# Kernel optimization log

Measured on AMD Instinct MI355X. Metric: run time of the kernel, lower is better.

## Reference

```python
import jax, jax.numpy as jnp
import numpy as np

D_MODEL = 1024
N_HEADS = 16
HEAD_DIM = D_MODEL // N_HEADS
HIDDEN = 4096
EPS = 1e-5


def setup_inputs() -> dict:
    key = jax.random.key(0)
    ks = jax.random.split(key, 16)
    s = 1.0 / np.sqrt(D_MODEL)
    sh = 1.0 / np.sqrt(HIDDEN)
    inp = {
        'x': jax.random.normal(ks[0], (4, 2048, D_MODEL), dtype=jnp.float32),
        'Wq': jax.random.normal(ks[1], (D_MODEL, D_MODEL), dtype=jnp.float32) * s,
        'bq': jnp.zeros((D_MODEL,), jnp.float32),
        'Wk': jax.random.normal(ks[2], (D_MODEL, D_MODEL), dtype=jnp.float32) * s,
        'bk': jnp.zeros((D_MODEL,), jnp.float32),
        'Wv': jax.random.normal(ks[3], (D_MODEL, D_MODEL), dtype=jnp.float32) * s,
        'bv': jnp.zeros((D_MODEL,), jnp.float32),
        'Wo': jax.random.normal(ks[4], (D_MODEL, D_MODEL), dtype=jnp.float32) * s,
        'bo': jnp.zeros((D_MODEL,), jnp.float32),
        'gamma1': jnp.ones((D_MODEL,), jnp.float32),
        'beta1': jnp.zeros((D_MODEL,), jnp.float32),
        'W1': jax.random.normal(ks[5], (D_MODEL, HIDDEN), dtype=jnp.float32) * s,
        'b1': jnp.zeros((HIDDEN,), jnp.float32),
        'W2': jax.random.normal(ks[6], (HIDDEN, D_MODEL), dtype=jnp.float32) * sh,
        'b2': jnp.zeros((D_MODEL,), jnp.float32),
        'gamma2': jnp.ones((D_MODEL,), jnp.float32),
        'beta2': jnp.zeros((D_MODEL,), jnp.float32),
    }
    return inp


def _layernorm(x, gamma, beta):
    mu = jnp.mean(x, axis=-1, keepdims=True)
    var = jnp.mean(jnp.square(x - mu), axis=-1, keepdims=True)
    return (x - mu) * jax.lax.rsqrt(var + EPS) * gamma + beta


def _encoder_layer(x, Wq, bq, Wk, bk, Wv, bv, Wo, bo, gamma1, beta1,
                   W1, b1, W2, b2, gamma2, beta2):
    B, S, _ = x.shape
    # projections -> [B, H, S, Dh]
    def split_heads(t):
        return t.reshape(B, S, N_HEADS, HEAD_DIM).transpose(0, 2, 1, 3)
    q = split_heads(x @ Wq + bq)
    k = split_heads(x @ Wk + bk)
    v = split_heads(x @ Wv + bv)
    scale = 1.0 / jnp.sqrt(jnp.float32(HEAD_DIM))
    scores = jnp.einsum('bhqd,bhkd->bhqk', q, k) * scale
    attn = jax.nn.softmax(scores, axis=-1)
    ctx = jnp.einsum('bhqk,bhkd->bhqd', attn, v)
    ctx = ctx.transpose(0, 2, 1, 3).reshape(B, S, D_MODEL)
    attn_out = ctx @ Wo + bo
    # post-norm residual 1
    h = _layernorm(x + attn_out, gamma1, beta1)
    # MLP with exact (erf) GELU, as torch F.gelu default
    mlp = jax.nn.gelu(h @ W1 + b1, approximate=False) @ W2 + b2
    return _layernorm(h + mlp, gamma2, beta2)


def reference(x, Wq, bq, Wk, bk, Wv, bv, Wo, bo, gamma1, beta1,
              W1, b1, W2, b2, gamma2, beta2):
    return _encoder_layer(x, Wq, bq, Wk, bk, Wv, bv, Wo, bo, gamma1, beta1,
                          W1, b1, W2, b2, gamma2, beta2)
```

## Files before the change

kernel.cpp:

```cpp
#include <hip/hip_runtime.h>
#include <cstdint>
#include <cstddef>

using u16 = unsigned short;
using bf16x8 = __attribute__((ext_vector_type(8))) short;
using f32x4  = __attribute__((ext_vector_type(4))) float;

__device__ __forceinline__ u16 f2bf(float f) {
    union { float f; unsigned u; } v; v.f = f;
    unsigned r = v.u + 0x7fffu + ((v.u >> 16) & 1u);
    return (u16)(r >> 16);
}

__device__ __forceinline__ float bf2f(u16 b) {
    union { unsigned u; float f; } v; v.u = (unsigned)b << 16;
    return v.f;
}

__device__ __forceinline__ unsigned cvtpk(float lo, float hi) {
    unsigned r;
    asm("v_cvt_pk_bf16_f32 %0, %1, %2" : "=v"(r) : "v"(lo), "v"(hi));
    return r;
}

__device__ __forceinline__ float fexp2(float x) {
    float r;
    asm("v_exp_f32 %0, %1" : "=v"(r) : "v"(x));
    return r;
}

__device__ __forceinline__ float gelu_f(float x) {
    const float t2 = fminf(x * fmaf(0.10294825f, x * x, 2.3022082f), 80.f);
    const float e  = fexp2(t2);
    return x * e * __frcp_rn(e + 1.0f);
}

__device__ __forceinline__ void gld_lds16(const void* g, void* l) {
    __builtin_amdgcn_global_load_lds(
        (__attribute__((address_space(1))) void*)g,
        (__attribute__((address_space(3))) void*)l, 16, 0, 0);
}

__device__ __forceinline__ f32x4 mfma16(bf16x8 a, bf16x8 b, f32x4 c) {
    return __builtin_amdgcn_mfma_f32_16x16x32_bf16(a, b, c, 0, 0, 0);
}

__global__ __launch_bounds__(256)
void cast_kernel(const float* __restrict__ in, u16* __restrict__ out, int n8) {
    int i = blockIdx.x * 256 + threadIdx.x;
    if (i >= n8) return;
    const float4* p = (const float4*)in;
    float4 a = p[i * 2], b = p[i * 2 + 1];
    ushort4 r0 = make_ushort4(f2bf(a.x), f2bf(a.y), f2bf(a.z), f2bf(a.w));
    ushort4 r1 = make_ushort4(f2bf(b.x), f2bf(b.y), f2bf(b.z), f2bf(b.w));
    ((ushort4*)out)[i * 2]     = r0;
    ((ushort4*)out)[i * 2 + 1] = r1;
}

__global__ __launch_bounds__(256)
void tcast_all_kernel(const float* __restrict__ Wq, const float* __restrict__ Wk,
                      const float* __restrict__ Wv, const float* __restrict__ Wo,
                      const float* __restrict__ W1, const float* __restrict__ W2,
                      u16* __restrict__ wqkvt, u16* __restrict__ wot,
                      u16* __restrict__ w1t, u16* __restrict__ w2t)
{
    const int g = blockIdx.x;
    const float* src; u16* dst; int K, N, ti; float scale = 1.0f;
    if (g < 1024)      { src = Wq; dst = wqkvt;               K = 1024; N = 1024; ti = g;        scale = 0.18033688011112042f; }
    else if (g < 2048) { src = Wk; dst = wqkvt + 1048576;     K = 1024; N = 1024; ti = g - 1024; }
    else if (g < 3072) { src = Wv; dst = wqkvt + 2097152;     K = 1024; N = 1024; ti = g - 2048; }
    else if (g < 4096) { src = Wo; dst = wot;                 K = 1024; N = 1024; ti = g - 3072; }
    else if (g < 8192) { src = W1; dst = w1t;                 K = 1024; N = 4096; ti = g - 4096; }
    else               { src = W2; dst = w2t;                 K = 4096; N = 1024; ti = g - 8192; }
    const int nt = N >> 5;
    const int bx = ti % nt, by = ti / nt;
    const int k0 = by * 32, n0 = bx * 32;

    __shared__ float tile[32][33];
    const int tx = threadIdx.x & 31, ty = threadIdx.x >> 5;
    #pragma unroll
    for (int r = 0; r < 4; ++r) {
        int k = ty * 4 + r;
        tile[k][tx] = src[(size_t)(k0 + k) * N + n0 + tx];
    }
    __syncthreads();
    const int kx = (threadIdx.x & 15) * 2;
    const int ny = threadIdx.x >> 4;
    #pragma unroll
    for (int r = 0; r < 2; ++r) {
        const int n = ny * 2 + r;
        ushort2 o = make_ushort2(f2bf(tile[kx][n] * scale),
                                 f2bf(tile[kx + 1][n] * scale));
        *(ushort2*)&dst[(size_t)(n0 + n) * K + k0 + kx] = o;
    }
}

__global__ __launch_bounds__(256)
void bias_concat_kernel(const float* __restrict__ bq, const float* __restrict__ bk,
                        const float* __restrict__ bv, float* __restrict__ out) {
    int i = blockIdx.x * 256 + threadIdx.x;
    if (i >= 3072) return;
    float v;
    if (i < 1024)      v = bq[i] * 0.18033688011112042f;
    else if (i < 2048) v = bk[i - 1024];
    else               v = bv[i - 2048];
    out[i] = v;
}

template <int BM, int EPI>
__global__ __launch_bounds__(512, 1)
void gemm_pipe_kernel(const u16* __restrict__ A, const u16* __restrict__ Bt,
                      const float* __restrict__ bias, void* __restrict__ Cout,
                      int M, int N, int K)
{
    constexpr int AH  = BM * 64;
    constexpr int BH  = 16384;
    constexpr int BUF = 2 * AH + 2 * BH;
    constexpr int LPA = BM / 128;
    constexpr int GRP = LPA + 2;
    constexpr int MR  = BM / 32;

    extern __shared__ char smem[];

    const int tid  = threadIdx.x;
    const int wid  = tid >> 6, lane = tid & 63;
    const int l15  = lane & 15, l4 = lane >> 4;
    const int wm   = wid >> 2, wn = wid & 3;

    const int nwg = gridDim.x;
    const int qx = nwg >> 3, rx = nwg & 7;
    const int orig = blockIdx.x;
    const int xcd = orig & 7, jx = orig >> 3;
    const int wgid = (xcd < rx ? xcd * (qx + 1) : rx * (qx + 1) + (xcd - rx) * qx) + jx;
    const int NTn = N / 256;
    const int m0 = (wgid / NTn) * BM;
    const int n0 = (wgid % NTn) * 256;

    const int q0 = tid >> 3, g0 = tid & 7;
    const int u0 = g0 ^ (q0 & 7);
    const int r0 = (q0 << 1) | (u0 >> 2), c80 = u0 & 3;
    const int q1 = q0 + 64;
    const int u1 = g0 ^ (q1 & 7);
    const int r1 = (q1 << 1) | (u1 >> 2), c81 = u1 & 3;
    const u16* aP0 = A  + (size_t)(m0 + r0) * K + c80 * 8;
    const u16* aP1 = A  + (size_t)(m0 + r1) * K + c81 * 8;
    const u16* bP0 = Bt + (size_t)(n0 + r0) * K + c80 * 8;
    const u16* bP1 = Bt + (size_t)(n0 + r1) * K + c81 * 8;
    const int NT = K >> 6;
    const int NTm1 = NT - 1;

    auto stageAB = [&](int tt, int kk, int sb) {
        const int kte = (tt << 6) + (kk << 5);
        char* da = smem + sb * BUF + kk * AH + tid * 16;
        gld_lds16(aP0 + kte, da);
        if constexpr (LPA == 2) gld_lds16(aP1 + kte, da + 8192);
        char* db = smem + sb * BUF + 2 * AH + kk * BH + tid * 16;
        gld_lds16(bP0 + kte, db);
        gld_lds16(bP1 + kte, db + 8192);
    };

    auto frag_off = [&](int row) -> int {
        const int q = row >> 1;
        const int u = ((row & 1) << 2) | l4;
        const int g = u ^ (q & 7);
        return q * 128 + g * 16;
    };

    f32x4 acc[MR][4];
    #pragma unroll
    for (int i = 0; i < MR; ++i)
        #pragma unroll
        for (int jj = 0; jj < 4; ++jj) acc[i][jj] = f32x4{0.f, 0.f, 0.f, 0.f};

    stageAB(0, 0, 0); stageAB(0, 1, 0); stageAB(1, 0, 1);
    if constexpr (GRP == 4) asm volatile("s_waitcnt vmcnt(8)" ::: "memory");
    else                    asm volatile("s_waitcnt vmcnt(6)" ::: "memory");
    __builtin_amdgcn_s_barrier();
    asm volatile("" ::: "memory");

    for (int t = 0; t < NT; ++t) {
        const char* buf = smem + (t & 1) * BUF;
        bf16x8 bfr[4], af[MR];

        #pragma unroll
        for (int kk = 0; kk < 2; ++kk) {
            #pragma unroll
            for (int fc = 0; fc < 4; ++fc)
                bfr[fc] = *(const bf16x8*)(buf + 2 * AH + kk * BH +
                                           frag_off(wn * 64 + fc * 16 + l15));
            #pragma unroll
            for (int i = 0; i < MR; ++i)
                af[i] = *(const bf16x8*)(buf + kk * AH +
                                         frag_off(wm * (BM / 2) + i * 16 + l15));
            if (kk == 0) {
                const int tt = (t + 1 <= NTm1) ? t + 1 : NTm1;
                stageAB(tt, 1, (t + 1) & 1);
            } else {
                const int tt = (t + 2 <= NTm1) ? t + 2 : NTm1;
                stageAB(tt, 0, t & 1);
            }
            if constexpr (GRP == 4) asm volatile("s_waitcnt vmcnt(8)" ::: "memory");
            else                    asm volatile("s_waitcnt vmcnt(6)" ::: "memory");
            __builtin_amdgcn_s_barrier();
            asm volatile("" ::: "memory");
            __builtin_amdgcn_s_setprio(1);
            #pragma unroll
            for (int i = 0; i < MR; ++i)
                #pragma unroll
                for (int fc = 0; fc < 4; ++fc)
                    acc[i][fc] = mfma16(af[i], bfr[fc], acc[i][fc]);
            __builtin_amdgcn_s_setprio(0);
            asm volatile("" ::: "memory");
        }
    }

    float bv[4];
    #pragma unroll
    for (int fc = 0; fc < 4; ++fc) bv[fc] = bias[n0 + wn * 64 + fc * 16 + l15];
    #pragma unroll
    for (int fr = 0; fr < MR; ++fr) {
        const int rowg = m0 + wm * (BM / 2) + fr * 16 + l4 * 4;
        #pragma unroll
        for (int fc = 0; fc < 4; ++fc) {
            const int colg = n0 + wn * 64 + fc * 16 + l15;
            #pragma unroll
            for (int r = 0; r < 4; ++r) {
                const float v = acc[fr][fc][r] + bv[fc];
                const size_t off = (size_t)(rowg + r) * N + colg;
                if (EPI == 0) ((u16*)Cout)[off] = f2bf(v);
                else          ((u16*)Cout)[off] = f2bf(gelu_f(v));
            }
        }
    }
}

__global__ __launch_bounds__(256)
void vtrans_kernel(const u16* __restrict__ QKV, u16* __restrict__ Vt) {
    __shared__ u16 tile[64][68];
    const int t  = threadIdx.x;
    const int st = blockIdx.x, bh = blockIdx.y;
    const int b  = bh >> 4, h = bh & 15;
    #pragma unroll
    for (int i = 0; i < 2; ++i) {
        int sl = i * 32 + (t >> 3);
        const u16* gp = QKV + ((size_t)b * 2048 + st * 64 + sl) * 3072 + 2048 + h * 64 + (t & 7) * 8;
        ushort4 a = *(const ushort4*)gp;
        ushort4 c = *(const ushort4*)(gp + 4);
        u16* lp = &tile[sl][(t & 7) * 8];
        *(ushort4*)lp       = a;
        *(ushort4*)(lp + 4) = c;
    }
    __syncthreads();
    #pragma unroll
    for (int i = 0; i < 2; ++i) {
        int d  = i * 32 + (t >> 3);
        int s8 = (t & 7) * 8;
        ushort4 o0, o1;
        o0.x = tile[s8 + 0][d]; o0.y = tile[s8 + 1][d]; o0.z = tile[s8 + 2][d]; o0.w = tile[s8 + 3][d];
        o1.x = tile[s8 + 4][d]; o1.y = tile[s8 + 5][d]; o1.z = tile[s8 + 6][d]; o1.w = tile[s8 + 7][d];
        u16* op = Vt + ((size_t)bh * 64 + d) * 2048 + st * 64 + s8;
        *(ushort4*)op       = o0;
        *(ushort4*)(op + 4) = o1;
    }
}

__global__ __launch_bounds__(512)
void attn_kernel(const u16* __restrict__ QKV, const u16* __restrict__ Vt,
                 u16* __restrict__ ctx)
{
    __shared__ u16 smem[24576];

    const int tid = threadIdx.x;
    const int wid = tid >> 6, lane = tid & 63;
    const int l15 = lane & 15, l4 = lane >> 4;
    const int sw  = l15 & 7;
    const int lr  = lane >> 3;
    const int gsrc = ((lane & 7) ^ lr) * 8;
    const int g   = blockIdx.x;
    const int bh  = (g & 7) | ((g >> 6) << 3);
    const int qt  = (g >> 3) & 7;
    const int b = bh >> 4, h = bh & 15;
    const size_t qrow0 = (size_t)b * 2048 + (size_t)qt * 256;

    u16* const K0 = smem + 16384;
    u16* const V0 = smem + 20480;
    u16* const K1 = smem;
    u16* const V1 = smem + 4096;

    const u16* Qbase = QKV + h * 64;
    const u16* Kbase = QKV + (size_t)b * 2048 * 3072 + 1024 + h * 64;
    const u16* Vbase = Vt + (size_t)bh * 64 * 2048;

    #pragma unroll
    for (int c = 0; c < 4; ++c) {
        const int chunk = wid * 4 + c;
        const int row = chunk * 8 + lr;
        gld_lds16(Qbase + (qrow0 + row) * 3072 + gsrc,
                  (char*)smem + chunk * 1024);
    }

    auto stage_kv = [&](int kt, u16* kb, u16* vb) {
        const int rho = wid * 8 + lr;
        const int krow = (rho & 32) + ((rho & 16) >> 2) + ((rho & 12) << 1) + (rho & 3);
        gld_lds16(Kbase + (size_t)(kt + krow) * 3072 + gsrc,
                  (char*)kb + wid * 1024);
        gld_lds16(Vbase + (size_t)rho * 2048 + kt + gsrc,
                  (char*)vb + wid * 1024);
    };

    stage_kv(0, K0, V0);
    __syncthreads();

    bf16x8 qf[2][2];
    #pragma unroll
    for (int mi = 0; mi < 2; ++mi)
        #pragma unroll
        for (int kk = 0; kk < 2; ++kk)
            qf[mi][kk] = *(const bf16x8*)
                &smem[(size_t)(wid * 32 + mi * 16 + l15) * 64 + (((kk * 4 + l4) ^ sw) * 8)];
    __syncthreads();

    f32x4 accO[2][4] = {};
    f32x4 accL[2] = {};
    const short one_bf = (short)0x3F80;
    const bf16x8 ones = {one_bf, one_bf, one_bf, one_bf,
                         one_bf, one_bf, one_bf, one_bf};

    union U4 { unsigned u[4]; bf16x8 v; };

    auto compute_tile = [&](const u16* kb, const u16* vb) {
        f32x4 st[2][4];
        #pragma unroll
        for (int mi = 0; mi < 2; ++mi)
            #pragma unroll
            for (int ni = 0; ni < 4; ++ni) st[mi][ni] = f32x4{0.f, 0.f, 0.f, 0.f};
        __builtin_amdgcn_s_setprio(1);
        #pragma unroll
        for (int ni = 0; ni < 4; ++ni) {
            bf16x8 kf0 = *(const bf16x8*)&kb[(ni * 16 + l15) * 64 + ((l4 ^ sw) * 8)];
            bf16x8 kf1 = *(const bf16x8*)&kb[(ni * 16 + l15) * 64 + (((4 + l4) ^ sw) * 8)];
            #pragma unroll
            for (int mi = 0; mi < 2; ++mi) {
                st[mi][ni] = mfma16(kf0, qf[mi][0], st[mi][ni]);
                st[mi][ni] = mfma16(kf1, qf[mi][1], st[mi][ni]);
            }
        }
        __builtin_amdgcn_s_setprio(0);

        U4 pb[2][2];
        #pragma unroll
        for (int mi = 0; mi < 2; ++mi) {
            float p[4][4];
            #pragma unroll
            for (int ni = 0; ni < 4; ++ni)
                #pragma unroll
                for (int r = 0; r < 4; ++r)
                    p[ni][r] = fexp2(st[mi][ni][r]);
            #pragma unroll
            for (int ni = 0; ni < 4; ++ni) {
                pb[mi][ni >> 1].u[(ni & 1) * 2 + 0] = cvtpk(p[ni][0], p[ni][1]);
                pb[mi][ni >> 1].u[(ni & 1) * 2 + 1] = cvtpk(p[ni][2], p[ni][3]);
            }
        }

        __builtin_amdgcn_s_setprio(1);
        #pragma unroll
        for (int mi = 0; mi < 2; ++mi) {
            accL[mi] = mfma16(ones, pb[mi][0].v, accL[mi]);
            accL[mi] = mfma16(ones, pb[mi][1].v, accL[mi]);
        }
        #pragma unroll
        for (int di = 0; di < 4; ++di) {
            bf16x8 vf0 = *(const bf16x8*)&vb[(di * 16 + l15) * 64 + ((l4 ^ sw) * 8)];
            bf16x8 vf1 = *(const bf16x8*)&vb[(di * 16 + l15) * 64 + (((4 + l4) ^ sw) * 8)];
            #pragma unroll
            for (int mi = 0; mi < 2; ++mi) {
                accO[mi][di] = mfma16(vf0, pb[mi][0].v, accO[mi][di]);
                accO[mi][di] = mfma16(vf1, pb[mi][1].v, accO[mi][di]);
            }
        }
        __builtin_amdgcn_s_setprio(0);
    };

    for (int it = 0; it < 32; it += 2) {
        if (it + 1 < 32) stage_kv((it + 1) * 64, K1, V1);
        compute_tile(K0, V0);
        __syncthreads();
        if (it + 2 < 32) stage_kv((it + 2) * 64, K0, V0);
        compute_tile(K1, V1);
        __syncthreads();
    }

    #pragma unroll
    for (int mi = 0; mi < 2; ++mi) {
        const float inv = 1.0f / accL[mi][0];
        const size_t q = qrow0 + wid * 32 + mi * 16 + l15;
        #pragma unroll
        for (int di = 0; di < 4; ++di) {
            uint2 w;
            w.x = cvtpk(accO[mi][di][0] * inv, accO[mi][di][1] * inv);
            w.y = cvtpk(accO[mi][di][2] * inv, accO[mi][di][3] * inv);
            *(uint2*)&ctx[q * 1024 + h * 64 + di * 16 + l4 * 4] = w;
        }
    }
}

__global__ __launch_bounds__(256)
void add_ln_kernel(const u16* __restrict__ X, const u16* __restrict__ Y,
                   const float* __restrict__ gamma, const float* __restrict__ beta,
                   float* __restrict__ outf, u16* __restrict__ outb)
{
    const int row = blockIdx.x;
    const int t = threadIdx.x;
    const ushort4 xb = ((const ushort4*)(X + (size_t)row * 1024))[t];
    const ushort4 yb = ((const ushort4*)(Y + (size_t)row * 1024))[t];
    const float v0 = bf2f(xb.x) + bf2f(yb.x);
    const float v1 = bf2f(xb.y) + bf2f(yb.y);
    const float v2 = bf2f(xb.z) + bf2f(yb.z);
    const float v3 = bf2f(xb.w) + bf2f(yb.w);
    float s  = v0 + v1 + v2 + v3;
    float ss = v0 * v0 + v1 * v1 + v2 * v2 + v3 * v3;
    #pragma unroll
    for (int m = 1; m < 64; m <<= 1) {
        s  += __shfl_xor(s, m, 64);
        ss += __shfl_xor(ss, m, 64);
    }
    __shared__ float red[8];
    const int wid = t >> 6, lane = t & 63;
    if (lane == 0) { red[wid] = s; red[4 + wid] = ss; }
    __syncthreads();
    s  = red[0] + red[1] + red[2] + red[3];
    ss = red[4] + red[5] + red[6] + red[7];
    const float mu  = s * (1.f / 1024.f);
    const float var = ss * (1.f / 1024.f) - mu * mu;
    const float inv = rsqrtf(var + 1e-5f);
    const float4 g  = ((const float4*)gamma)[t];
    const float4 bb = ((const float4*)beta)[t];
    float4 o;
    o.x = (v0 - mu) * inv * g.x + bb.x;
    o.y = (v1 - mu) * inv * g.y + bb.y;
    o.z = (v2 - mu) * inv * g.z + bb.z;
    o.w = (v3 - mu) * inv * g.w + bb.w;
    if (outf != nullptr)
        ((float4*)(outf + (size_t)row * 1024))[t] = o;
    if (outb != nullptr) {
        ushort4 ob = make_ushort4(f2bf(o.x), f2bf(o.y), f2bf(o.z), f2bf(o.w));
        ((ushort4*)(outb + (size_t)row * 1024))[t] = ob;
    }
}

extern "C" void kernel_launch(void* const* d_in, const int* in_sizes, int n_in,
                              void* d_out, int out_size, void* d_ws, size_t ws_size,
                              hipStream_t stream)
{
    (void)in_sizes; (void)n_in; (void)out_size; (void)ws_size;
    const float* x   = (const float*)d_in[0];
    const float* Wq  = (const float*)d_in[1];
    const float* bq  = (const float*)d_in[2];
    const float* Wk  = (const float*)d_in[3];
    const float* bk  = (const float*)d_in[4];
    const float* Wv  = (const float*)d_in[5];
    const float* bv  = (const float*)d_in[6];
    const float* Wo  = (const float*)d_in[7];
    const float* bo  = (const float*)d_in[8];
    const float* g1  = (const float*)d_in[9];
    const float* be1 = (const float*)d_in[10];
    const float* W1  = (const float*)d_in[11];
    const float* b1  = (const float*)d_in[12];
    const float* W2  = (const float*)d_in[13];
    const float* b2  = (const float*)d_in[14];
    const float* g2  = (const float*)d_in[15];
    const float* be2 = (const float*)d_in[16];

    constexpr int M = 8192;
    constexpr int D = 1024;
    constexpr int F = 4096;

    char* ws = (char*)d_ws;
    size_t off = 0;
    auto nxt = [&](size_t bytes) -> char* {
        char* p = ws + off;
        off += (bytes + 255) & ~(size_t)255;
        return p;
    };
    u16*   xb    = (u16*)nxt((size_t)M * D * 2);
    u16*   wqkvt = (u16*)nxt((size_t)3 * D * D * 2);
    u16*   wot   = (u16*)nxt((size_t)D * D * 2);
    u16*   w1t   = (u16*)nxt((size_t)F * D * 2);
    u16*   w2t   = (u16*)nxt((size_t)D * F * 2);
    float* bqkv  = (float*)nxt(3072 * 4);
    u16*   qkv   = (u16*)nxt((size_t)M * 3 * D * 2);
    u16*   Vtb   = (u16*)nxt((size_t)M * D * 2);
    u16*   ctx   = (u16*)nxt((size_t)M * D * 2);
    u16*   attn  = (u16*)nxt((size_t)M * D * 2);
    u16*   hb    = (u16*)nxt((size_t)M * D * 2);
    u16*   t1    = qkv;
    u16*   mlp   = attn;

    cast_kernel<<<dim3(M * D / 8 / 256), dim3(256), 0, stream>>>(x, xb, M * D / 8);
    tcast_all_kernel<<<dim3(12288), dim3(256), 0, stream>>>(
        Wq, Wk, Wv, Wo, W1, W2, wqkvt, wot, w1t, w2t);
    bias_concat_kernel<<<dim3(12), dim3(256), 0, stream>>>(bq, bk, bv, bqkv);

    constexpr size_t LDS128 = 2 * (2 * 128 * 64 + 2 * 16384);
    constexpr size_t LDS256 = 2 * (2 * 256 * 64 + 2 * 16384);

    gemm_pipe_kernel<128, 0><<<dim3((M / 128) * (3 * D / 256)), dim3(512), LDS128, stream>>>(
        xb, wqkvt, bqkv, qkv, M, 3 * D, D);

    vtrans_kernel<<<dim3(2048 / 64, 64), dim3(256), 0, stream>>>(qkv, Vtb);
    attn_kernel<<<dim3(512), dim3(512), 0, stream>>>(qkv, Vtb, ctx);

    gemm_pipe_kernel<128, 0><<<dim3((M / 128) * (D / 256)), dim3(512), LDS128, stream>>>(
        ctx, wot, bo, attn, M, D, D);
    add_ln_kernel<<<dim3(M), dim3(256), 0, stream>>>(xb, attn, g1, be1, nullptr, hb);

    gemm_pipe_kernel<256, 2><<<dim3((M / 256) * (F / 256)), dim3(512), LDS256, stream>>>(
        hb, w1t, b1, t1, M, F, D);
    gemm_pipe_kernel<128, 0><<<dim3((M / 128) * (D / 256)), dim3(512), LDS128, stream>>>(
        t1, w2t, b2, mlp, M, D, F);
    add_ln_kernel<<<dim3(M), dim3(256), 0, stream>>>(hb, mlp, g2, be2, (float*)d_out, nullptr);
}
```

Before: 356.6 us.

## Add small-LDS BK=32 GEMM kernel for 128-row GEMMs and fuse x cast into prepass

Adds a new GEMM kernel with a K-step of 32 and a double-buffered 48KB LDS footprint, launch-bounded for up to four workgroups per CU. It replaces the deeper-pipelined 128-row GEMM for the QKV, output and W2 projections. The aim is to hide latency through occupancy rather than a multi-stage software pipeline. The x-to-bf16 cast is also folded into the weight transpose-cast kernel, which saves one launch. The tradeoff is half the K per barrier, so synchronisation overhead rises, and the epilogue uses scalar 2-byte stores.

```diff
diff --git a/kernel.cpp b/kernel.cpp
--- a/kernel.cpp
+++ b/kernel.cpp
@@ -46,25 +46,25 @@
 }
 
 __global__ __launch_bounds__(256)
-void cast_kernel(const float* __restrict__ in, u16* __restrict__ out, int n8) {
-    int i = blockIdx.x * 256 + threadIdx.x;
-    if (i >= n8) return;
-    const float4* p = (const float4*)in;
-    float4 a = p[i * 2], b = p[i * 2 + 1];
-    ushort4 r0 = make_ushort4(f2bf(a.x), f2bf(a.y), f2bf(a.z), f2bf(a.w));
-    ushort4 r1 = make_ushort4(f2bf(b.x), f2bf(b.y), f2bf(b.z), f2bf(b.w));
-    ((ushort4*)out)[i * 2]     = r0;
-    ((ushort4*)out)[i * 2 + 1] = r1;
-}
-
-__global__ __launch_bounds__(256)
-void tcast_all_kernel(const float* __restrict__ Wq, const float* __restrict__ Wk,
-                      const float* __restrict__ Wv, const float* __restrict__ Wo,
-                      const float* __restrict__ W1, const float* __restrict__ W2,
-                      u16* __restrict__ wqkvt, u16* __restrict__ wot,
-                      u16* __restrict__ w1t, u16* __restrict__ w2t)
+void prepass_kernel(const float* __restrict__ Wq, const float* __restrict__ Wk,
+                    const float* __restrict__ Wv, const float* __restrict__ Wo,
+                    const float* __restrict__ W1, const float* __restrict__ W2,
+                    const float* __restrict__ x,
+                    u16* __restrict__ wqkvt, u16* __restrict__ wot,
+                    u16* __restrict__ w1t, u16* __restrict__ w2t,
+                    u16* __restrict__ xb)
 {
     const int g = blockIdx.x;
+    if (g >= 12288) {
+        const int i = (g - 12288) * 256 + threadIdx.x;
+        const float4* p = (const float4*)x;
+        float4 a = p[i * 2], b = p[i * 2 + 1];
+        ushort4 r0 = make_ushort4(f2bf(a.x), f2bf(a.y), f2bf(a.z), f2bf(a.w));
+        ushort4 r1 = make_ushort4(f2bf(b.x), f2bf(b.y), f2bf(b.z), f2bf(b.w));
+        ((ushort4*)xb)[i * 2]     = r0;
+        ((ushort4*)xb)[i * 2 + 1] = r1;
+        return;
+    }
     const float* src; u16* dst; int K, N, ti; float scale = 1.0f;
     if (g < 1024)      { src = Wq; dst = wqkvt;               K = 1024; N = 1024; ti = g;        scale = 0.18033688011112042f; }
     else if (g < 2048) { src = Wk; dst = wqkvt + 1048576;     K = 1024; N = 1024; ti = g - 1024; }
@@ -105,6 +105,114 @@
     else if (i < 2048) v = bk[i - 1024];
     else               v = bv[i - 2048];
     out[i] = v;
+}
+
+template <int EPI>
+__global__ __launch_bounds__(512, 4)
+void gemm_bk32_kernel(const u16* __restrict__ A, const u16* __restrict__ Bt,
+                      const float* __restrict__ bias, void* __restrict__ Cout,
+                      int M, int N, int K)
+{
+    constexpr int AH  = 8192;
+    constexpr int BH  = 16384;
+    constexpr int BUF = AH + BH;
+
+    extern __shared__ char smem[];
+
+    const int tid  = threadIdx.x;
+    const int wid  = tid >> 6, lane = tid & 63;
+    const int l15  = lane & 15, l4 = lane >> 4;
+    const int wm   = wid >> 2, wn = wid & 3;
+
+    const int nwg = gridDim.x;
+    const int qx = nwg >> 3, rx = nwg & 7;
+    const int orig = blockIdx.x;
+    const int xcd = orig & 7, jx = orig >> 3;
+    const int wgid = (xcd < rx ? xcd * (qx + 1) : rx * (qx + 1) + (xcd - rx) * qx) + jx;
+    const int NTn = N / 256;
+    const int m0 = (wgid / NTn) * 128;
+    const int n0 = (wgid % NTn) * 256;
+
+    const int q0 = tid >> 3, g0 = tid & 7;
+    const int u0 = g0 ^ (q0 & 7);
+    const int r0 = (q0 << 1) | (u0 >> 2), c80 = u0 & 3;
+    const int q1 = q0 + 64;
+    const int u1 = g0 ^ (q1 & 7);
+    const int r1 = (q1 << 1) | (u1 >> 2), c81 = u1 & 3;
+    const u16* aP0 = A  + (size_t)(m0 + r0) * K + c80 * 8;
+    const u16* bP0 = Bt + (size_t)(n0 + r0) * K + c80 * 8;
+    const u16* bP1 = Bt + (size_t)(n0 + r1) * K + c81 * 8;
+    const int NT = K >> 5;
+
+    auto stage = [&](int tt, int sb) {
+        const int kte = tt << 5;
+        gld_lds16(aP0 + kte, smem + sb * BUF + tid * 16);
+        char* db = smem + sb * BUF + AH + tid * 16;
+        gld_lds16(bP0 + kte, db);
+        gld_lds16(bP1 + kte, db + 8192);
+    };
+
+    auto frag_off = [&](int row) -> int {
+        const int q = row >> 1;
+        const int u = ((row & 1) << 2) | l4;
+        const int g = u ^ (q & 7);
+        return q * 128 + g * 16;
+    };
+
+    f32x4 acc[4][4];
+    #pragma unroll
+    for (int i = 0; i < 4; ++i)
+        #pragma unroll
+        for (int jj = 0; jj < 4; ++jj) acc[i][jj] = f32x4{0.f, 0.f, 0.f, 0.f};
+
+    stage(0, 0);
+
+    for (int t = 0; t < NT; ++t) {
+        const int tn = (t + 1 < NT) ? t + 1 : t;
+        stage(tn, (t + 1) & 1);
+        asm volatile("s_waitcnt vmcnt(3)" ::: "memory");
+        __builtin_amdgcn_s_barrier();
+        asm volatile("" ::: "memory");
+
+        const char* buf = smem + (t & 1) * BUF;
+        bf16x8 bfr[4], af[4];
+        #pragma unroll
+        for (int fc = 0; fc < 4; ++fc)
+            bfr[fc] = *(const bf16x8*)(buf + AH + frag_off(wn * 64 + fc * 16 + l15));
+        #pragma unroll
+        for (int i = 0; i < 4; ++i)
+            af[i] = *(const bf16x8*)(buf + frag_off(wm * 64 + i * 16 + l15));
+
+        __builtin_amdgcn_s_setprio(1);
+        #pragma unroll
+        for (int i = 0; i < 4; ++i)
+            #pragma unroll
+            for (int fc = 0; fc < 4; ++fc)
+                acc[i][fc] = mfma16(af[i], bfr[fc], acc[i][fc]);
+        __builtin_amdgcn_s_setprio(0);
+        asm volatile("" ::: "memory");
+        __builtin_amdgcn_s_barrier();
+        asm volatile("" ::: "memory");
+    }
+
+    float bv[4];
+    #pragma unroll
+    for (int fc = 0; fc < 4; ++fc) bv[fc] = bias[n0 + wn * 64 + fc * 16 + l15];
+    #pragma unroll
+    for (int fr = 0; fr < 4; ++fr) {
+        const int rowg = m0 + wm * 64 + fr * 16 + l4 * 4;
+        #pragma unroll
+        for (int fc = 0; fc < 4; ++fc) {
+            const int colg = n0 + wn * 64 + fc * 16 + l15;
+            #pragma unroll
+            for (int r = 0; r < 4; ++r) {
+                const float v = acc[fr][fc][r] + bv[fc];
+                const size_t off = (size_t)(rowg + r) * N + colg;
+                if (EPI == 0) ((u16*)Cout)[off] = f2bf(v);
+                else          ((u16*)Cout)[off] = f2bf(gelu_f(v));
+            }
+        }
+    }
 }
 
 template <int BM, int EPI>
@@ -497,27 +605,26 @@
     u16*   t1    = qkv;
     u16*   mlp   = attn;
 
-    cast_kernel<<<dim3(M * D / 8 / 256), dim3(256), 0, stream>>>(x, xb, M * D / 8);
-    tcast_all_kernel<<<dim3(12288), dim3(256), 0, stream>>>(
-        Wq, Wk, Wv, Wo, W1, W2, wqkvt, wot, w1t, w2t);
+    prepass_kernel<<<dim3(16384), dim3(256), 0, stream>>>(
+        Wq, Wk, Wv, Wo, W1, W2, x, wqkvt, wot, w1t, w2t, xb);
     bias_concat_kernel<<<dim3(12), dim3(256), 0, stream>>>(bq, bk, bv, bqkv);
 
-    constexpr size_t LDS128 = 2 * (2 * 128 * 64 + 2 * 16384);
+    constexpr size_t LDSB32 = 2 * (8192 + 16384);
     constexpr size_t LDS256 = 2 * (2 * 256 * 64 + 2 * 16384);
 
-    gemm_pipe_kernel<128, 0><<<dim3((M / 128) * (3 * D / 256)), dim3(512), LDS128, stream>>>(
+    gemm_bk32_kernel<0><<<dim3((M / 128) * (3 * D / 256)), dim3(512), LDSB32, stream>>>(
         xb, wqkvt, bqkv, qkv, M, 3 * D, D);
 
     vtrans_kernel<<<dim3(2048 / 64, 64), dim3(256), 0, stream>>>(qkv, Vtb);
     attn_kernel<<<dim3(512), dim3(512), 0, stream>>>(qkv, Vtb, ctx);
 
-    gemm_pipe_kernel<128, 0><<<dim3((M / 128) * (D / 256)), dim3(512), LDS128, stream>>>(
+    gemm_bk32_kernel<0><<<dim3((M / 128) * (D / 256)), dim3(512), LDSB32, stream>>>(
         ctx, wot, bo, attn, M, D, D);
     add_ln_kernel<<<dim3(M), dim3(256), 0, stream>>>(xb, attn, g1, be1, nullptr, hb);
 
     gemm_pipe_kernel<256, 2><<<dim3((M / 256) * (F / 256)), dim3(512), LDS256, stream>>>(
         hb, w1t, b1, t1, M, F, D);
-    gemm_pipe_kernel<128, 0><<<dim3((M / 128) * (D / 256)), dim3(512), LDS128, stream>>>(
+    gemm_bk32_kernel<0><<<dim3((M / 128) * (D / 256)), dim3(512), LDSB32, stream>>>(
         t1, w2t, b2, mlp, M, D, F);
     add_ln_kernel<<<dim3(M), dim3(256), 0, stream>>>(hb, mlp, g2, be2, (float*)d_out, nullptr);
 }
```

Measured after the change: 364.0 us. +2.1%, slower.
